# Performance work log

Hardware: AMD Instinct MI355X
Metric: run time of the kernel (lower is better)

The kernel has to match this reference:

```python
import jax, jax.numpy as jnp
import numpy as np

T, N, DOBS, V = 32, 64, 16, 16
E = DOBS * V          # embedding_size = 256
HID = 1024            # GRU / model hidden size
A = 32                # num_options
S = 32                # planning_steps
HP = 8                # planning_horizon
INF = 1e8


def setup_inputs() -> dict:
    key = jax.random.key(0)
    ks = jax.random.split(key, 16)
    sc = 0.02
    norm = lambda k, sh: jax.random.normal(k, sh, dtype=jnp.float32) * sc
    return {
        "obs": jax.random.randint(ks[0], (T, N, DOBS), 0, V, dtype=jnp.int32),
        "P": jax.random.randint(ks[1], (S, N), 0, A, dtype=jnp.int32),
        "embed1": norm(ks[2], (V, V)),
        "Wih": norm(ks[3], (3 * HID, E)),
        "Whh": norm(ks[4], (3 * HID, HID)),
        "bih": jnp.zeros(3 * HID, jnp.float32),
        "bhh": jnp.zeros(3 * HID, jnp.float32),
        "We2": norm(ks[5], (E, HID)),
        "be2": jnp.zeros(E, jnp.float32),
        "Ws": norm(ks[6], (1, E)),
        "bs": jnp.zeros(1, jnp.float32),
        "Wc": norm(ks[7], (A, E)),
        "bc": jnp.zeros(A, jnp.float32),
        "Wm1": norm(ks[8], (HID, A * E)),
        "bm1": jnp.zeros(HID, jnp.float32),
        "Wm2": norm(ks[9], (E, HID)),
        "bm2": jnp.zeros(E, jnp.float32),
        "embed_opt": norm(ks[10], (A, A)),
    }


def _gru(xs, Wih, Whh, bih, bhh):
    # torch nn.GRU equations, single layer, h0 = 0
    def step(h, x):
        gi = x @ Wih.T + bih
        gh = h @ Whh.T + bhh
        ir, iz, inn = jnp.split(gi, 3, axis=-1)
        hr, hz, hn = jnp.split(gh, 3, axis=-1)
        r = jax.nn.sigmoid(ir + hr)
        z = jax.nn.sigmoid(iz + hz)
        n = jnp.tanh(inn + r * hn)
        h = (1 - z) * n + z * h
        return h, h
    h0 = jnp.zeros((xs.shape[1], Whh.shape[1]), xs.dtype)
    _, hs = jax.lax.scan(step, h0, xs)
    return hs  # (T, N, HID)


def _model(x, a_emb, Wm1, bm1, Wm2, bm2):
    # Product -> Flatten -> relu -> Linear(E*A, HID) -> relu -> Linear(HID, E)
    prod = a_emb[..., :, None] * x[..., None, :]            # (B, A, E)
    flat = jax.nn.relu(prod.reshape(prod.shape[0], A * E))  # (B, A*E)
    h = jax.nn.relu(flat @ Wm1.T + bm1)                     # (B, HID)
    return h @ Wm2.T + bm2                                  # (B, E)


def _forward(obs, P, embed1, Wih, Whh, bih, bhh, We2, be2, Ws, bs, Wc, bc,
             Wm1, bm1, Wm2, bm2, embed_opt):
    emb = embed1[obs].reshape(T, N, E)                      # per-dim embed, flattened
    Hs = _gru(emb, Wih, Whh, bih, bhh)                      # (T, N, HID)
    ar = jnp.arange(N)

    X0 = jnp.zeros((N, HP, E), emb.dtype).at[:, 0].set(Hs[0] @ We2.T + be2)
    I0 = jnp.zeros(N, jnp.int32)
    logits0 = jnp.zeros((N, A), emb.dtype)
    pa0 = jnp.zeros((N, HP), jnp.int32)

    def plan_step(carry, a):
        I, X, logits, pa = carry
        x = X[ar, I]                                        # pointer gather (N, E)
        xa = jax.nn.relu(x)
        sharp = xa @ Ws.T + bs                              # (N, 1)
        vals = xa @ Wc.T + bc                               # (N, A)
        is_new = jnp.all(logits == 0, axis=-1)
        sl = jnp.where(is_new[:, None], sharp * vals, logits)
        logits = sl - INF * jax.nn.one_hot(a, A, dtype=sl.dtype)
        v_a = jnp.take_along_axis(vals, a[:, None], axis=1)[:, 0]
        push = v_a > 0
        pa = pa.at[ar, I].set(a)                            # pointer scatter
        x_next = _model(x, embed_opt[a], Wm1, bm1, Wm2, bm2)
        I_up = jnp.minimum(I + 1, HP - 1)
        X = X.at[ar, I_up].set(jnp.where(push[:, None], x_next, X[ar, I_up]))
        I = jnp.where(push, I_up, jnp.maximum(I - 1, 0))
        return (I, X, logits, pa), sl

    (_, X, _, planned_actions), search_logits = jax.lax.scan(
        plan_step, (I0, X0, logits0, pa0), P)               # search_logits (S, N, A)

    # time loop (vectorized): model loss against next embedded state
    prev = jnp.concatenate([emb[-1:], emb[:-1]], axis=0)    # inputs[t-1] (torch wrap at t=0)
    model_out = _model(prev.reshape(T * N, E),
                       embed_opt[P].reshape(T * N, A),
                       Wm1, bm1, Wm2, bm2).reshape(T, N, E)
    model_loss = (model_out - jax.lax.stop_gradient(emb)) ** 2

    eps = 1e-8
    emb_n = emb / (jnp.linalg.norm(emb, axis=-1, keepdims=True) + eps)
    X_n = X / (jnp.linalg.norm(X, axis=-1, keepdims=True) + eps)
    cos = jnp.einsum('tne,nhe->tnh', emb_n, X_n)            # cosine sim vs plan buffer
    sharp_t = jax.nn.relu(emb) @ Ws.T + bs                  # (T, N, 1)
    logp = jax.nn.log_softmax(sharp_t * cos, axis=-1)
    embed_loss = jnp.sum(jnp.exp(logp) * logp, axis=-1)     # -entropy, (T, N)

    value = jnp.take_along_axis(search_logits, P[:, :, None], axis=2)[..., 0]  # (T, N)
    return search_logits, planned_actions, X, value, model_loss, embed_loss


def reference(obs, P, embed1, Wih, Whh, bih, bhh, We2, be2, Ws, bs, Wc, bc,
              Wm1, bm1, Wm2, bm2, embed_opt):
    return _forward(obs, P, embed1, Wih, Whh, bih, bhh, We2, be2, Ws, bs,
                    Wc, bc, Wm1, bm1, Wm2, bm2, embed_opt)
```

## Files before the change

### kernel.cpp

```cpp
#include <hip/hip_runtime.h>

constexpr int CT = 32;
constexpr int CN = 64;
constexpr int CE = 256;
constexpr int CHID = 1024;
constexpr int CA = 32;
constexpr int CS = 32;
constexpr int CHP = 8;
constexpr int TN = CT * CN;

constexpr size_t O_SL  = 0;
constexpr size_t O_PA  = 65536;
constexpr size_t O_X   = 66048;
constexpr size_t O_VAL = 197120;
constexpr size_t O_ML  = 199168;
constexpr size_t O_EL  = 723456;

constexpr size_t B_EMB    = 0;
constexpr size_t B_H1     = 2u * 1024 * 1024;
constexpr size_t B_FLG    = 3584u * 1024;
constexpr size_t B_CNTTL  = B_FLG + 64 * 1024;
constexpr size_t B_LISTTL = B_CNTTL + 4 * 1024;
constexpr size_t B_R32    = 4u * 1024 * 1024;
constexpr size_t B_WE2T   = B_R32;
constexpr size_t B_WM1T   = B_R32;
constexpr size_t B_XSTL   = B_R32;
constexpr size_t B_HBIG   = B_R32 + 4u * 1024 * 1024;
constexpr size_t B_PARTTL = B_R32 + 12u * 1024 * 1024;
constexpr size_t B_PART3  = B_R32;
constexpr size_t B_WM2T   = B_R32 + 28u * 1024 * 1024;
constexpr size_t B_WPM    = B_R32 + 32u * 1024 * 1024;

constexpr int SI_FLAG = 0, SI_I = 1, SI_PUSH = 2, SI_IUP = 3;

__device__ __forceinline__ void fma4(float4& a, float s, const float4& w) {
  a.x = fmaf(s, w.x, a.x); a.y = fmaf(s, w.y, a.y);
  a.z = fmaf(s, w.z, a.z); a.w = fmaf(s, w.w, a.w);
}

__device__ __forceinline__ float gld(const float* p) {
  return __hip_atomic_load(p, __ATOMIC_RELAXED, __HIP_MEMORY_SCOPE_AGENT);
}
__device__ __forceinline__ void gst(float* p, float v) {
  __hip_atomic_store(p, v, __ATOMIC_RELAXED, __HIP_MEMORY_SCOPE_AGENT);
}
__device__ __forceinline__ int gldi(const int* p) {
  return __hip_atomic_load(p, __ATOMIC_RELAXED, __HIP_MEMORY_SCOPE_AGENT);
}
__device__ __forceinline__ void gsti(int* p, int v) {
  __hip_atomic_store(p, v, __ATOMIC_RELAXED, __HIP_MEMORY_SCOPE_AGENT);
}
__device__ __forceinline__ void waitst() {
  asm volatile("s_waitcnt vmcnt(0)" ::: "memory");
}

__global__ void init_kernel(float* __restrict__ out, int* __restrict__ flg,
                            int* __restrict__ cnt_tl) {
  int idx = blockIdx.x * 256 + threadIdx.x;
  if (idx < 131584) out[O_PA + idx] = 0.f;
  if (idx < CN * 8 * 16) flg[idx] = 0;
  if (idx < CA) cnt_tl[idx] = 0;
}

__global__ void emb_kernel(const int* __restrict__ obs, const float* __restrict__ embed1,
                           float* __restrict__ emb) {
  int idx = blockIdx.x * 256 + threadIdx.x;
  int b = idx >> 5, k8 = idx & 31;
  int e0 = k8 * 8;
  int d = e0 >> 4;
  int o = obs[b * 16 + d];
  const float* src = embed1 + o * 16 + (e0 & 15);
  float4 v0 = *(const float4*)src;
  float4 v1 = *(const float4*)(src + 4);
  float* dst = emb + (size_t)b * CE + e0;
  *(float4*)dst = v0;
  *(float4*)(dst + 4) = v1;
}

__global__ void h1_kernel(const float* __restrict__ emb, const float* __restrict__ Wih,
                          const float* __restrict__ bih, const float* __restrict__ bhh,
                          float* __restrict__ h1) {
  int t = threadIdx.x, bid = blockIdx.x;
  int n = t & 63, j = bid * 4 + (t >> 6);
  const float* x = emb + (size_t)n * CE;
  const float* wr = Wih + (size_t)j * CE;
  const float* wz = Wih + (size_t)(CHID + j) * CE;
  const float* wn = Wih + (size_t)(2 * CHID + j) * CE;
  float ar = 0.f, az = 0.f, an = 0.f;
  #pragma unroll 4
  for (int e = 0; e < CE; ++e) {
    float xe = x[e];
    ar += xe * wr[e]; az += xe * wz[e]; an += xe * wn[e];
  }
  ar += bih[j] + bhh[j];
  az += bih[CHID + j] + bhh[CHID + j];
  float r = 1.f / (1.f + expf(-ar));
  float z = 1.f / (1.f + expf(-az));
  float nn = tanhf(an + bih[2 * CHID + j] + r * bhh[2 * CHID + j]);
  h1[(size_t)n * CHID + j] = (1.f - z) * nn;
}

__global__ void trans_kernel(const float* __restrict__ in, float* __restrict__ out,
                             int R, int C) {
  __shared__ float tile[64][65];
  int tj = threadIdx.x & 63, tg = threadIdx.x >> 6;
  int cb = blockIdx.x * 64, rb = blockIdx.y * 64;
  #pragma unroll
  for (int i = 0; i < 16; ++i) {
    int r = tg * 16 + i;
    tile[r][tj] = in[(size_t)(rb + r) * C + cb + tj];
  }
  __syncthreads();
  #pragma unroll
  for (int i = 0; i < 16; ++i) {
    int c2 = tg * 16 + i;
    out[(size_t)(cb + c2) * R + rb + tj] = tile[tj][c2];
  }
}

__global__ void x0_kernel(const float* __restrict__ h1, const float* __restrict__ We2T,
                          const float* __restrict__ be2, float* __restrict__ Xout) {
  int et = blockIdx.x, n = blockIdx.y, t = threadIdx.x;
  int el = t & 63, kq = t >> 6;
  __shared__ float hr[1024];
  __shared__ float sred2[4][64];
  for (int idx = t; idx < 1024; idx += 256) hr[idx] = h1[(size_t)n * CHID + idx];
  __syncthreads();
  int e = et * 64 + el;
  float acc = 0.f;
  for (int k = kq * 256; k < kq * 256 + 256; ++k) acc += hr[k] * We2T[(size_t)k * CE + e];
  sred2[kq][el] = acc;
  __syncthreads();
  if (t < 64) {
    float s2 = sred2[0][t] + sred2[1][t] + sred2[2][t] + sred2[3][t] + be2[et * 64 + t];
    Xout[(size_t)(n * CHP) * CE + et * 64 + t] = s2;
  }
}

__global__ void wpm_kernel(const float* __restrict__ Wm1T, const float* __restrict__ eo,
                           float* __restrict__ Wpm) {
  int e = blockIdx.x, jt = blockIdx.y, t = threadIdx.x;
  int j = jt * 256 + t;
  __shared__ float rp[CA * CA], rm[CA * CA];
  for (int idx = t; idx < CA * CA; idx += 256) {
    float v = eo[idx];
    rp[idx] = fmaxf(v, 0.f);
    rm[idx] = fmaxf(-v, 0.f);
  }
  __syncthreads();
  float w[32];
  #pragma unroll
  for (int a = 0; a < 32; ++a) w[a] = Wm1T[(size_t)(a * 256 + e) * CHID + j];
  for (int o = 0; o < 32; ++o) {
    float sp = 0.f, sm = 0.f;
    #pragma unroll
    for (int a = 0; a < 32; ++a) {
      float wa = w[a];
      sp += rp[o * 32 + a] * wa;
      sm += rm[o * 32 + a] * wa;
    }
    Wpm[((size_t)o * 512 + e) * CHID + j] = sp;
    Wpm[((size_t)o * 512 + 256 + e) * CHID + j] = sm;
  }
}

__global__ void tllists_kernel(const int* __restrict__ P, int* __restrict__ cnt_tl,
                               int* __restrict__ list_tl) {
  int b = blockIdx.x * 256 + threadIdx.x;
  if (b >= TN) return;
  int a = P[b];
  int slot = atomicAdd(&cnt_tl[a], 1);
  list_tl[a * 256 + slot] = b;
}

__global__ void xstl_kernel(const float* __restrict__ emb, float* __restrict__ xs) {
  int idx = blockIdx.x * 256 + threadIdx.x;
  int b = idx >> 9, k = idx & 511;
  int e = k & 255;
  int bp = (b < CN) ? (b + (CT - 1) * CN) : (b - CN);
  float v = emb[(size_t)bp * CE + e];
  xs[idx] = (k < 256) ? fmaxf(v, 0.f) : fmaxf(-v, 0.f);
}

__global__ __launch_bounds__(256) void l1_kernel(
    const float* __restrict__ Wpm, const float* __restrict__ xs,
    const float* __restrict__ bm1, const int* __restrict__ cnt,
    const int* __restrict__ list, int listStride, float* __restrict__ hout) {
  int o = blockIdx.x, jt = blockIdx.y;
  int c = cnt[o];
  if (c <= 0) return;
  __shared__ __align__(16) float sbuf[8192];
  __shared__ int srows[8];
  int t = threadIdx.x;
  int jl = t & 31, kq = t >> 5;
  int jb = jt * 128;
  const float* wb = Wpm + (size_t)o * (512 * CHID) + jb + jl * 4;
  for (int g = blockIdx.z; g * 8 < c; g += gridDim.z) {
    int base = g * 8;
    int nr = min(8, c - base);
    if (t < 8) srows[t] = (t < nr) ? list[o * listStride + base + t] : -1;
    __syncthreads();
    for (int idx = t; idx < 4096; idx += 256) {
      int row = srows[idx >> 9];
      sbuf[idx] = (row >= 0) ? xs[(size_t)row * 512 + (idx & 511)] : 0.f;
    }
    __syncthreads();
    float4 acc[8];
    #pragma unroll
    for (int r = 0; r < 8; ++r) acc[r] = make_float4(0.f, 0.f, 0.f, 0.f);
    int kbase = kq * 64;
    for (int k4 = 0; k4 < 64; k4 += 4) {
      int k = kbase + k4;
      float4 w0 = *(const float4*)(wb + (size_t)(k + 0) * CHID);
      float4 w1 = *(const float4*)(wb + (size_t)(k + 1) * CHID);
      float4 w2 = *(const float4*)(wb + (size_t)(k + 2) * CHID);
      float4 w3 = *(const float4*)(wb + (size_t)(k + 3) * CHID);
      #pragma unroll
      for (int r = 0; r < 8; ++r) {
        float4 xv = *(const float4*)&sbuf[r * 512 + k];
        fma4(acc[r], xv.x, w0); fma4(acc[r], xv.y, w1);
        fma4(acc[r], xv.z, w2); fma4(acc[r], xv.w, w3);
      }
    }
    __syncthreads();
    #pragma unroll
    for (int r = 0; r < 8; ++r)
      *(float4*)&sbuf[(kq * 8 + r) * 128 + jl * 4] = acc[r];
    __syncthreads();
    for (int idx = t; idx < 1024; idx += 256) {
      int r = idx >> 7, jc = idx & 127;
      float s = 0.f;
      #pragma unroll
      for (int q = 0; q < 8; ++q) s += sbuf[(q * 8 + r) * 128 + jc];
      int row = srows[r];
      if (row >= 0)
        hout[(size_t)row * CHID + jb + jc] = fmaxf(s + bm1[jb + jc], 0.f);
    }
    __syncthreads();
  }
}

__global__ __launch_bounds__(256) void l2big_kernel(const float* __restrict__ h,
    const float* __restrict__ Wm2T, float* __restrict__ part) {
  int kq = blockIdx.x, rg = blockIdx.y, t = threadIdx.x;
  int rb = rg * 32, kb = kq * 128;
  __shared__ __align__(16) float hl[4096];
  for (int idx = t; idx < 4096; idx += 256)
    hl[idx] = h[(size_t)(rb + (idx >> 7)) * CHID + kb + (idx & 127)];
  __syncthreads();
  float acc[32];
  #pragma unroll
  for (int r = 0; r < 32; ++r) acc[r] = 0.f;
  for (int kk = 0; kk < 128; kk += 4) {
    float w0 = Wm2T[(size_t)(kb + kk + 0) * CE + t];
    float w1 = Wm2T[(size_t)(kb + kk + 1) * CE + t];
    float w2 = Wm2T[(size_t)(kb + kk + 2) * CE + t];
    float w3 = Wm2T[(size_t)(kb + kk + 3) * CE + t];
    #pragma unroll
    for (int r = 0; r < 32; ++r) {
      float4 hv = *(const float4*)&hl[r * 128 + kk];
      acc[r] += hv.x * w0 + hv.y * w1 + hv.z * w2 + hv.w * w3;
    }
  }
  #pragma unroll
  for (int r = 0; r < 32; ++r)
    part[((size_t)(rb + r) * 8 + kq) * CE + t] = acc[r];
}

__global__ void ml_kernel(const float* __restrict__ part, const float* __restrict__ bm2,
                          const float* __restrict__ emb, float* __restrict__ ML) {
  int idx = blockIdx.x * 256 + threadIdx.x;
  int b = idx >> 8, e = idx & 255;
  float outv = bm2[e];
  #pragma unroll
  for (int q = 0; q < 8; ++q) outv += part[((size_t)b * 8 + q) * CE + e];
  float d = outv - emb[idx];
  ML[idx] = d * d;
}

__global__ __launch_bounds__(512) void plan2_kernel(
    const float* __restrict__ Wpm, const float* __restrict__ Wm2T,
    const float* __restrict__ bm1g, const int* __restrict__ P,
    const float* __restrict__ Wsg, const float* __restrict__ bsg,
    const float* __restrict__ Wcg, const float* __restrict__ bcg,
    const float* __restrict__ bm2, float* __restrict__ Xout,
    float* __restrict__ SLout, float* __restrict__ VALout,
    float* __restrict__ PAout, int* __restrict__ flg,
    float* __restrict__ part_db) {
  __shared__ float Xlds[CHP * CE];
  __shared__ int   skidx[256];
  __shared__ float sxv[256];
  __shared__ float sh[128];
  __shared__ __align__(16) float red[2048];
  __shared__ float sx[256];
  __shared__ float sred[8];
  __shared__ float svals[32];
  __shared__ float sxtra[2];
  __shared__ int   sint[4];
  __shared__ float logits_s[32];

  int bid = blockIdx.x, t = threadIdx.x;
  int n = bid >> 3, q = bid & 7;
  int jb = q * 128;
  int c2 = t >> 3, g = t & 7;
  int jq = t & 31, kg = t >> 5;
  int e2 = t & 255, hf = t >> 8;

  for (int idx = t; idx < CHP * CE; idx += 512)
    Xlds[idx] = Xout[(size_t)n * (CHP * CE) + idx];
  if (t < 32) logits_s[t] = 0.f;
  if (t < 4) sint[t] = 0;
  __syncthreads();

  for (int s = 0; s <= CS; ++s) {
    float wsv = 0.f, bm2v = 0.f, bcv = 0.f, bsv = bsg[0];
    float wcv[32];
    if (t < 256) {
      wsv = Wsg[t]; bm2v = bm2[t];
      #pragma unroll
      for (int i = 0; i < 32; ++i) wcv[i] = Wcg[c2 * CE + g * 32 + i];
    }
    if (t < CA) bcv = bcg[t];

    if (s > 0) {
      if (t < 8) {
        const int* fp = &flg[(n * 8 + t) * 16];
        while (gldi(fp) < s) __builtin_amdgcn_s_sleep(1);
      }
      __syncthreads();
      if (sint[SI_PUSH]) {
        int Iup = sint[SI_IUP];
        if (t < 256) {
          float outv = bm2v;
          #pragma unroll
          for (int qq = 0; qq < 8; ++qq)
            outv += gld(&part_db[(((size_t)(s - 1) * CN + n) * 8 + qq) * CE + t]);
          Xlds[Iup * CE + t] = outv;
          if (q == 0) Xout[((size_t)(n * CHP) + Iup) * CE + t] = outv;
          sx[t] = outv;
        }
        if (t == 0) sint[SI_I] = Iup;
      } else {
        int I0 = sint[SI_I];
        int Inew = (I0 - 1 > 0) ? I0 - 1 : 0;
        if (t < 256) sx[t] = Xlds[Inew * CE + t];
        if (t == 0) sint[SI_I] = Inew;
      }
      if (s == CS) break;
    } else {
      if (t < 256) sx[t] = Xlds[t];
      if (t == 0) sint[SI_I] = 0;
    }
    __syncthreads();
    int I = sint[SI_I];

    if (t < 256) {
      float xv = sx[t];
      float xa = fmaxf(xv, 0.f);
      skidx[t] = (xv > 0.f) ? t : 256 + t;
      sxv[t] = fabsf(xv);
      float v = xa * wsv;
      #pragma unroll
      for (int off = 32; off > 0; off >>= 1) v += __shfl_down(v, off, 64);
      if ((t & 63) == 0) sred[t >> 6] = v;
      float pv = 0.f;
      #pragma unroll 4
      for (int i = 0; i < 32; ++i)
        pv += fmaxf(sx[g * 32 + i], 0.f) * wcv[i];
      pv += __shfl_down(pv, 4, 8);
      pv += __shfl_down(pv, 2, 8);
      pv += __shfl_down(pv, 1, 8);
      if (g == 0) svals[c2] = pv + bcv;
    }
    __syncthreads();
    if (t == 0) {
      sxtra[0] = sred[0] + sred[1] + sred[2] + sred[3] + bsv;
      sint[SI_FLAG] = 1;
    }
    __syncthreads();
    if (t < CA && logits_s[t] != 0.f) sint[SI_FLAG] = 0;
    __syncthreads();
    int a = P[s * CN + n];
    if (t < CA) {
      float v = svals[t];
      float slv = sint[SI_FLAG] ? sxtra[0] * v : logits_s[t];
      if (q == 0) SLout[(size_t)(s * CN + n) * CA + t] = slv;
      logits_s[t] = slv - (t == a ? 1e8f : 0.f);
      if (t == a) {
        if (q == 0) { VALout[s * CN + n] = slv; PAout[n * CHP + I] = (float)a; }
        sint[SI_PUSH] = (v > 0.f) ? 1 : 0;
        sint[SI_IUP] = (I + 1 < CHP - 1) ? I + 1 : CHP - 1;
      }
    }
    __syncthreads();

    if (sint[SI_PUSH]) {
      const float* wbase = Wpm + (size_t)a * (512 * CHID) + jb + jq * 4;
      float4 acc; acc.x = acc.y = acc.z = acc.w = 0.f;
      #pragma unroll 8
      for (int ii = 0; ii < 16; ++ii) {
        int e = kg * 16 + ii;
        float4 wv = *(const float4*)(wbase + (size_t)skidx[e] * CHID);
        fma4(acc, sxv[e], wv);
      }
      *(float4*)&red[kg * 128 + jq * 4] = acc;
      __syncthreads();
      if (t < 128) {
        float s1 = 0.f;
        #pragma unroll
        for (int gg = 0; gg < 16; ++gg) s1 += red[gg * 128 + t];
        sh[t] = fmaxf(s1 + bm1g[jb + t], 0.f);
      }
      __syncthreads();
      {
        const float* w2 = Wm2T + (size_t)(jb + hf * 64) * CE + e2;
        float a2 = 0.f;
        #pragma unroll 8
        for (int kl = 0; kl < 64; ++kl)
          a2 = fmaf(sh[hf * 64 + kl], w2[(size_t)kl * CE], a2);
        red[hf * 256 + e2] = a2;
      }
      __syncthreads();
      if (t < 256) {
        gst(&part_db[(((size_t)s * CN + n) * 8 + q) * CE + t],
            red[t] + red[256 + t]);
      }
    }
    __syncthreads();
    if (t == 0) {
      waitst();
      gsti(&flg[(n * 8 + q) * 16], s + 1);
    }
    __syncthreads();
  }
}

__global__ void el_kernel(const float* __restrict__ emb, const float* __restrict__ Xout,
                          const float* __restrict__ Ws, const float* __restrict__ bsp,
                          float* __restrict__ EL) {
  int tn = blockIdx.x;
  int n = tn & 63;
  int t = threadIdx.x, h = t >> 5, l = t & 31;
  const float* er = emb + (size_t)tn * CE;
  const float* xr = Xout + ((size_t)(n * CHP) + h) * CE;
  float pd = 0.f, px = 0.f, pe = 0.f, ps = 0.f;
  #pragma unroll
  for (int i = 0; i < 8; ++i) {
    int e = l * 8 + i;
    float ev = er[e], xv2 = xr[e];
    pd += ev * xv2; px += xv2 * xv2; pe += ev * ev; ps += fmaxf(ev, 0.f) * Ws[e];
  }
  #pragma unroll
  for (int off = 16; off > 0; off >>= 1) {
    pd += __shfl_down(pd, off, 32);
    px += __shfl_down(px, off, 32);
    pe += __shfl_down(pe, off, 32);
    ps += __shfl_down(ps, off, 32);
  }
  __shared__ float sdot[8], snx[8];
  __shared__ float sne, ssh;
  if (l == 0) {
    sdot[h] = pd;
    snx[h] = sqrtf(px);
    if (h == 0) { sne = sqrtf(pe); ssh = ps + bsp[0]; }
  }
  __syncthreads();
  if (t == 0) {
    const float eps = 1e-8f;
    float y[8];
    float m = -1e30f;
    #pragma unroll
    for (int hh = 0; hh < 8; ++hh) {
      float cs = sdot[hh] / ((sne + eps) * (snx[hh] + eps));
      y[hh] = ssh * cs;
      m = fmaxf(m, y[hh]);
    }
    float sum = 0.f;
    #pragma unroll
    for (int hh = 0; hh < 8; ++hh) sum += expf(y[hh] - m);
    float lse = logf(sum);
    float el = 0.f;
    #pragma unroll
    for (int hh = 0; hh < 8; ++hh) {
      float lp = y[hh] - m - lse;
      el += expf(lp) * lp;
    }
    EL[tn] = el;
  }
}

extern "C" void kernel_launch(void* const* d_in, const int* in_sizes, int n_in,
                              void* d_out, int out_size, void* d_ws, size_t ws_size,
                              hipStream_t stream) {
  (void)in_sizes; (void)n_in; (void)out_size; (void)ws_size;
  const int*   obs    = (const int*)d_in[0];
  const int*   P      = (const int*)d_in[1];
  const float* embed1 = (const float*)d_in[2];
  const float* Wih    = (const float*)d_in[3];
  const float* bih    = (const float*)d_in[5];
  const float* bhh    = (const float*)d_in[6];
  const float* We2    = (const float*)d_in[7];
  const float* be2    = (const float*)d_in[8];
  const float* Ws     = (const float*)d_in[9];
  const float* bs     = (const float*)d_in[10];
  const float* Wc     = (const float*)d_in[11];
  const float* bc     = (const float*)d_in[12];
  const float* Wm1    = (const float*)d_in[13];
  const float* bm1    = (const float*)d_in[14];
  const float* Wm2    = (const float*)d_in[15];
  const float* bm2    = (const float*)d_in[16];
  const float* eo     = (const float*)d_in[17];
  float* out = (float*)d_out;
  char*  ws  = (char*)d_ws;

  float* emb    = (float*)(ws + B_EMB);
  float* h1     = (float*)(ws + B_H1);
  float* part_db= (float*)(ws + B_PART3);
  int*   flg    = (int*)(ws + B_FLG);
  int*   cnttl  = (int*)(ws + B_CNTTL);
  int*   listtl = (int*)(ws + B_LISTTL);
  float* we2t   = (float*)(ws + B_WE2T);
  float* wm1t   = (float*)(ws + B_WM1T);
  float* xstl   = (float*)(ws + B_XSTL);
  float* hbig   = (float*)(ws + B_HBIG);
  float* parttl = (float*)(ws + B_PARTTL);
  float* wm2t   = (float*)(ws + B_WM2T);
  float* wpm    = (float*)(ws + B_WPM);

  dim3 thr(256);
  init_kernel<<<dim3(514), thr, 0, stream>>>(out, flg, cnttl);
  emb_kernel<<<dim3(256), thr, 0, stream>>>(obs, embed1, emb);
  h1_kernel<<<dim3(256), thr, 0, stream>>>(emb, Wih, bih, bhh, h1);
  trans_kernel<<<dim3(16, 4), thr, 0, stream>>>(We2, we2t, CE, CHID);
  x0_kernel<<<dim3(4, 64), thr, 0, stream>>>(h1, we2t, be2, out + O_X);
  trans_kernel<<<dim3(128, 16), thr, 0, stream>>>(Wm1, wm1t, CHID, CA * CE);
  wpm_kernel<<<dim3(256, 4), thr, 0, stream>>>(wm1t, eo, wpm);
  trans_kernel<<<dim3(16, 4), thr, 0, stream>>>(Wm2, wm2t, CE, CHID);
  tllists_kernel<<<dim3(8), thr, 0, stream>>>(P, cnttl, listtl);
  xstl_kernel<<<dim3(4096), thr, 0, stream>>>(emb, xstl);
  l1_kernel<<<dim3(32, 8, 8), thr, 0, stream>>>(wpm, xstl, bm1, cnttl, listtl, 256, hbig);
  l2big_kernel<<<dim3(8, 64), thr, 0, stream>>>(hbig, wm2t, parttl);
  ml_kernel<<<dim3(2048), thr, 0, stream>>>(parttl, bm2, emb, out + O_ML);
  plan2_kernel<<<dim3(512), dim3(512), 0, stream>>>(
      wpm, wm2t, bm1, P, Ws, bs, Wc, bc, bm2,
      out + O_X, out + O_SL, out + O_VAL, out + O_PA, flg, part_db);
  el_kernel<<<dim3(2048), thr, 0, stream>>>(emb, out + O_X, Ws, bs, out + O_EL);
}
```

Before: 481.5 us.

## Fuse model layer-2 into layer-1 kernel and streamline planning-step barriers

The separate second-layer GEMM kernel and its hidden-activation buffer are removed. Each layer-1 block now applies the Wm2 projection to its 8-row hidden tile and writes per-jt partial sums directly. In the sequential planning kernel, the Wpm row loads are issued early into registers before the reductions, so their latency overlaps with the logit computation. Several shared-memory flag barriers are replaced by a wave ballot and lighter LDS-only barriers, and every thread now spins on the cross-block flags. The trade-offs are more register pressure, repeated Wm2T reads per row group in the fused kernel, and reliance on the custom barrier being correct.

New measurement: 635.0 us. 1.32x slower.

```diff
diff --git a/kernel.cpp b/kernel.cpp
--- a/kernel.cpp
+++ b/kernel.cpp
@@ -25,7 +25,6 @@
 constexpr size_t B_WE2T   = B_R32;
 constexpr size_t B_WM1T   = B_R32;
 constexpr size_t B_XSTL   = B_R32;
-constexpr size_t B_HBIG   = B_R32 + 4u * 1024 * 1024;
 constexpr size_t B_PARTTL = B_R32 + 12u * 1024 * 1024;
 constexpr size_t B_PART3  = B_R32;
 constexpr size_t B_WM2T   = B_R32 + 28u * 1024 * 1024;
@@ -52,6 +51,11 @@
 }
 __device__ __forceinline__ void waitst() {
   asm volatile("s_waitcnt vmcnt(0)" ::: "memory");
+}
+__device__ __forceinline__ void syncL() {
+  asm volatile("s_waitcnt lgkmcnt(0)" ::: "memory");
+  __builtin_amdgcn_s_barrier();
+  __builtin_amdgcn_sched_barrier(0);
 }
 
 __global__ void init_kernel(float* __restrict__ out, int* __restrict__ flg,
@@ -182,14 +186,16 @@
   xs[idx] = (k < 256) ? fmaxf(v, 0.f) : fmaxf(-v, 0.f);
 }
 
-__global__ __launch_bounds__(256) void l1_kernel(
+__global__ __launch_bounds__(256) void tl_kernel(
     const float* __restrict__ Wpm, const float* __restrict__ xs,
-    const float* __restrict__ bm1, const int* __restrict__ cnt,
-    const int* __restrict__ list, int listStride, float* __restrict__ hout) {
+    const float* __restrict__ bm1, const float* __restrict__ Wm2T,
+    const int* __restrict__ cnt, const int* __restrict__ list,
+    int listStride, float* __restrict__ part) {
   int o = blockIdx.x, jt = blockIdx.y;
   int c = cnt[o];
   if (c <= 0) return;
   __shared__ __align__(16) float sbuf[8192];
+  __shared__ __align__(16) float hh[8 * 128];
   __shared__ int srows[8];
   int t = threadIdx.x;
   int jl = t & 31, kq = t >> 5;
@@ -229,42 +235,32 @@
     __syncthreads();
     for (int idx = t; idx < 1024; idx += 256) {
       int r = idx >> 7, jc = idx & 127;
-      float s = 0.f;
-      #pragma unroll
-      for (int q = 0; q < 8; ++q) s += sbuf[(q * 8 + r) * 128 + jc];
-      int row = srows[r];
-      if (row >= 0)
-        hout[(size_t)row * CHID + jb + jc] = fmaxf(s + bm1[jb + jc], 0.f);
-    }
-    __syncthreads();
-  }
-}
-
-__global__ __launch_bounds__(256) void l2big_kernel(const float* __restrict__ h,
-    const float* __restrict__ Wm2T, float* __restrict__ part) {
-  int kq = blockIdx.x, rg = blockIdx.y, t = threadIdx.x;
-  int rb = rg * 32, kb = kq * 128;
-  __shared__ __align__(16) float hl[4096];
-  for (int idx = t; idx < 4096; idx += 256)
-    hl[idx] = h[(size_t)(rb + (idx >> 7)) * CHID + kb + (idx & 127)];
-  __syncthreads();
-  float acc[32];
-  #pragma unroll
-  for (int r = 0; r < 32; ++r) acc[r] = 0.f;
-  for (int kk = 0; kk < 128; kk += 4) {
-    float w0 = Wm2T[(size_t)(kb + kk + 0) * CE + t];
-    float w1 = Wm2T[(size_t)(kb + kk + 1) * CE + t];
-    float w2 = Wm2T[(size_t)(kb + kk + 2) * CE + t];
-    float w3 = Wm2T[(size_t)(kb + kk + 3) * CE + t];
-    #pragma unroll
-    for (int r = 0; r < 32; ++r) {
-      float4 hv = *(const float4*)&hl[r * 128 + kk];
-      acc[r] += hv.x * w0 + hv.y * w1 + hv.z * w2 + hv.w * w3;
-    }
-  }
-  #pragma unroll
-  for (int r = 0; r < 32; ++r)
-    part[((size_t)(rb + r) * 8 + kq) * CE + t] = acc[r];
+      float ssum = 0.f;
+      #pragma unroll
+      for (int q8 = 0; q8 < 8; ++q8) ssum += sbuf[(q8 * 8 + r) * 128 + jc];
+      hh[r * 128 + jc] = fmaxf(ssum + bm1[jb + jc], 0.f);
+    }
+    __syncthreads();
+    float acc2[8];
+    #pragma unroll
+    for (int r = 0; r < 8; ++r) acc2[r] = 0.f;
+    for (int jj = 0; jj < 128; jj += 4) {
+      float w0 = Wm2T[(size_t)(jb + jj + 0) * CE + t];
+      float w1 = Wm2T[(size_t)(jb + jj + 1) * CE + t];
+      float w2 = Wm2T[(size_t)(jb + jj + 2) * CE + t];
+      float w3 = Wm2T[(size_t)(jb + jj + 3) * CE + t];
+      #pragma unroll
+      for (int r = 0; r < 8; ++r) {
+        float4 hv = *(const float4*)&hh[r * 128 + jj];
+        acc2[r] += hv.x * w0 + hv.y * w1 + hv.z * w2 + hv.w * w3;
+      }
+    }
+    #pragma unroll
+    for (int r = 0; r < 8; ++r)
+      if (srows[r] >= 0)
+        part[((size_t)srows[r] * 8 + jt) * CE + t] = acc2[r];
+    __syncthreads();
+  }
 }
 
 __global__ void ml_kernel(const float* __restrict__ part, const float* __restrict__ bm2,
@@ -288,14 +284,11 @@
     float* __restrict__ PAout, int* __restrict__ flg,
     float* __restrict__ part_db) {
   __shared__ float Xlds[CHP * CE];
-  __shared__ int   skidx[256];
-  __shared__ float sxv[256];
   __shared__ float sh[128];
   __shared__ __align__(16) float red[2048];
   __shared__ float sx[256];
   __shared__ float sred[8];
   __shared__ float svals[32];
-  __shared__ float sxtra[2];
   __shared__ int   sint[4];
   __shared__ float logits_s[32];
 
@@ -323,11 +316,11 @@
     if (t < CA) bcv = bcg[t];
 
     if (s > 0) {
-      if (t < 8) {
-        const int* fp = &flg[(n * 8 + t) * 16];
+      #pragma unroll
+      for (int f = 0; f < 8; ++f) {
+        const int* fp = &flg[(n * 8 + f) * 16];
         while (gldi(fp) < s) __builtin_amdgcn_s_sleep(1);
       }
-      __syncthreads();
       if (sint[SI_PUSH]) {
         int Iup = sint[SI_IUP];
         if (t < 256) {
@@ -351,15 +344,24 @@
       if (t < 256) sx[t] = Xlds[t];
       if (t == 0) sint[SI_I] = 0;
     }
-    __syncthreads();
+    syncL();
     int I = sint[SI_I];
+    int a = P[s * CN + n];
+
+    const float* wbase = Wpm + (size_t)a * (512 * CHID) + jb + jq * 4;
+    float4 wr[16];
+    float  xa16[16];
+    #pragma unroll
+    for (int ii = 0; ii < 16; ++ii) {
+      int e = kg * 16 + ii;
+      float xv = sx[e];
+      xa16[ii] = fabsf(xv);
+      int row = (xv > 0.f) ? e : 256 + e;
+      wr[ii] = *(const float4*)(wbase + (size_t)row * CHID);
+    }
 
     if (t < 256) {
-      float xv = sx[t];
-      float xa = fmaxf(xv, 0.f);
-      skidx[t] = (xv > 0.f) ? t : 256 + t;
-      sxv[t] = fabsf(xv);
-      float v = xa * wsv;
+      float v = fmaxf(sx[t], 0.f) * wsv;
       #pragma unroll
       for (int off = 32; off > 0; off >>= 1) v += __shfl_down(v, off, 64);
       if ((t & 63) == 0) sred[t >> 6] = v;
@@ -372,18 +374,13 @@
       pv += __shfl_down(pv, 1, 8);
       if (g == 0) svals[c2] = pv + bcv;
     }
-    __syncthreads();
-    if (t == 0) {
-      sxtra[0] = sred[0] + sred[1] + sred[2] + sred[3] + bsv;
-      sint[SI_FLAG] = 1;
-    }
-    __syncthreads();
-    if (t < CA && logits_s[t] != 0.f) sint[SI_FLAG] = 0;
-    __syncthreads();
-    int a = P[s * CN + n];
+    syncL();
     if (t < CA) {
+      float sharp = sred[0] + sred[1] + sred[2] + sred[3] + bsv;
+      bool nz = (logits_s[t] != 0.f);
+      unsigned long long bal = __ballot(nz);
       float v = svals[t];
-      float slv = sint[SI_FLAG] ? sxtra[0] * v : logits_s[t];
+      float slv = (bal == 0ull) ? sharp * v : logits_s[t];
       if (q == 0) SLout[(size_t)(s * CN + n) * CA + t] = slv;
       logits_s[t] = slv - (t == a ? 1e8f : 0.f);
       if (t == a) {
@@ -392,26 +389,21 @@
         sint[SI_IUP] = (I + 1 < CHP - 1) ? I + 1 : CHP - 1;
       }
     }
-    __syncthreads();
+    syncL();
 
     if (sint[SI_PUSH]) {
-      const float* wbase = Wpm + (size_t)a * (512 * CHID) + jb + jq * 4;
       float4 acc; acc.x = acc.y = acc.z = acc.w = 0.f;
-      #pragma unroll 8
-      for (int ii = 0; ii < 16; ++ii) {
-        int e = kg * 16 + ii;
-        float4 wv = *(const float4*)(wbase + (size_t)skidx[e] * CHID);
-        fma4(acc, sxv[e], wv);
-      }
+      #pragma unroll
+      for (int ii = 0; ii < 16; ++ii) fma4(acc, xa16[ii], wr[ii]);
       *(float4*)&red[kg * 128 + jq * 4] = acc;
-      __syncthreads();
+      syncL();
       if (t < 128) {
         float s1 = 0.f;
         #pragma unroll
         for (int gg = 0; gg < 16; ++gg) s1 += red[gg * 128 + t];
         sh[t] = fmaxf(s1 + bm1g[jb + t], 0.f);
       }
-      __syncthreads();
+      syncL();
       {
         const float* w2 = Wm2T + (size_t)(jb + hf * 64) * CE + e2;
         float a2 = 0.f;
@@ -420,7 +412,7 @@
           a2 = fmaf(sh[hf * 64 + kl], w2[(size_t)kl * CE], a2);
         red[hf * 256 + e2] = a2;
       }
-      __syncthreads();
+      syncL();
       if (t < 256) {
         gst(&part_db[(((size_t)s * CN + n) * 8 + q) * CE + t],
             red[t] + red[256 + t]);
@@ -522,7 +514,6 @@
   float* we2t   = (float*)(ws + B_WE2T);
   float* wm1t   = (float*)(ws + B_WM1T);
   float* xstl   = (float*)(ws + B_XSTL);
-  float* hbig   = (float*)(ws + B_HBIG);
   float* parttl = (float*)(ws + B_PARTTL);
   float* wm2t   = (float*)(ws + B_WM2T);
   float* wpm    = (float*)(ws + B_WPM);
@@ -538,8 +529,8 @@
   trans_kernel<<<dim3(16, 4), thr, 0, stream>>>(Wm2, wm2t, CE, CHID);
   tllists_kernel<<<dim3(8), thr, 0, stream>>>(P, cnttl, listtl);
   xstl_kernel<<<dim3(4096), thr, 0, stream>>>(emb, xstl);
-  l1_kernel<<<dim3(32, 8, 8), thr, 0, stream>>>(wpm, xstl, bm1, cnttl, listtl, 256, hbig);
-  l2big_kernel<<<dim3(8, 64), thr, 0, stream>>>(hbig, wm2t, parttl);
+  tl_kernel<<<dim3(32, 8, 8), thr, 0, stream>>>(wpm, xstl, bm1, wm2t,
+                                                cnttl, listtl, 256, parttl);
   ml_kernel<<<dim3(2048), thr, 0, stream>>>(parttl, bm2, emb, out + O_ML);
   plan2_kernel<<<dim3(512), dim3(512), 0, stream>>>(
       wpm, wm2t, bm1, P, Ws, bs, Wc, bc, bm2,
```
